# Kernel tuning notes

Hardware: AMD Instinct MI355X
Metric: run time of the kernel (lower is better)

Reference implementation:

```python
import jax, jax.numpy as jnp
import numpy as np

TEMPERATURE = 0.07


def setup_inputs() -> dict:
    key = jax.random.key(0)
    k1, k2, k3 = jax.random.split(key, 3)
    b, num_proposals, num_phrases, f = 128, 100, 16, 512
    img_features = jax.random.normal(k1, (b, num_proposals, f), dtype=jnp.float32)
    text_features = jax.random.normal(k2, (b, num_phrases, f), dtype=jnp.float32)
    labels = jax.random.randint(k3, (b, b), 0, 2, dtype=jnp.int64)
    return {"img_features": img_features, "text_features": text_features, "labels": labels}


def reference(img_features, text_features, labels):
    # att_matrix[b,d,t,i] = <text[b,t,:], img[d,i,:]>
    att_matrix = jnp.einsum('btf,dif->bdti', text_features, img_features)
    argmax_box = att_matrix.max(axis=3)        # [b, d, t]  max over proposals
    score_matrix = argmax_box.mean(axis=2)     # [b, d]     mean over phrases
    score_exp = jnp.exp(score_matrix / TEMPERATURE)
    return score_exp
```

## Files before the change

kernel.cpp:

```cpp
#include <hip/hip_runtime.h>
#include <hip/hip_bf16.h>
#include <stdint.h>


typedef __attribute__((ext_vector_type(8))) short bf16x8;
typedef __attribute__((ext_vector_type(4))) float f32x4;

constexpr int Bb = 128;
constexpr int P  = 100;
constexpr int T  = 16;
constexpr int F  = 512;
constexpr float TEMP = 0.07f;

constexpr int BM = 128;
constexpr int BN = 128;
constexpr int BK = 64;

__device__ __forceinline__ unsigned short f2bf(float x) {
  union { float f; uint32_t u; } c; c.f = x;
  uint32_t r = (c.u + 0x7FFFu + ((c.u >> 16) & 1u)) >> 16;
  return (unsigned short)r;
}

__global__ void cvt_kernel(const float4* __restrict__ img, const float4* __restrict__ txt,
                           ushort4* __restrict__ imgb, ushort4* __restrict__ txtb,
                           int nimg4, int ntxt4) {
  const int stride = gridDim.x * blockDim.x;
  for (int i = blockIdx.x * blockDim.x + threadIdx.x; i < nimg4; i += stride) {
    float4 v = img[i];
    ushort4 o = { f2bf(v.x), f2bf(v.y), f2bf(v.z), f2bf(v.w) };
    imgb[i] = o;
  }
  for (int i = blockIdx.x * blockDim.x + threadIdx.x; i < ntxt4; i += stride) {
    float4 v = txt[i];
    ushort4 o = { f2bf(v.x), f2bf(v.y), f2bf(v.z), f2bf(v.w) };
    txtb[i] = o;
  }
}

template<bool FUSED>
__global__ __launch_bounds__(256)
void score_kernel(const void* __restrict__ imgp, const void* __restrict__ txtp,
                  float* __restrict__ out) {
  __shared__ __align__(16) unsigned short As[BM * BK];
  __shared__ __align__(16) unsigned short Bs[BN * BK];
  __shared__ float red[BM][2];

  const int d    = blockIdx.x;
  const int b0   = blockIdx.y * (BM / T);
  const int tid  = threadIdx.x;
  const int lane = tid & 63;
  const int w    = tid >> 6;
  const int q    = lane >> 4;
  const int n    = lane & 15;
  const int mh   = w & 1;
  const int nh   = w >> 1;

  f32x4 acc[4][4] = {};

  for (int kk = 0; kk < F; kk += BK) {
    if constexpr (!FUSED) {
      const unsigned short* gi = (const unsigned short*)imgp;
      const unsigned short* gt = (const unsigned short*)txtp;
      const int sub = lane >> 3;
      const int col = (((lane & 7) ^ sub) & 7) * 8;
      #pragma unroll
      for (int rr = 0; rr < 4; rr++) {
        const int c   = rr * 4 + w;
        const int row = c * 8 + sub;
        const unsigned short* ga = gt + (size_t)(b0 * T + row) * F + kk + col;
        __builtin_amdgcn_global_load_lds(
            (const __attribute__((address_space(1))) void*)ga,
            (__attribute__((address_space(3))) void*)&As[c * 512], 16, 0, 0);
        const int prow = row < P ? row : 0;
        const unsigned short* gb = gi + ((size_t)d * P + prow) * F + kk + col;
        __builtin_amdgcn_global_load_lds(
            (const __attribute__((address_space(1))) void*)gb,
            (__attribute__((address_space(3))) void*)&Bs[c * 512], 16, 0, 0);
      }
    } else {
      const float* gi = (const float*)imgp;
      const float* gt = (const float*)txtp;
      #pragma unroll
      for (int s = 0; s < 8; s++) {
        const int slot = s * 256 + tid;
        const int row  = slot >> 4;
        const int half = slot & 15;
        const int colg = half * 4;
        const int kc   = half >> 1;
        const int cols = ((kc ^ (row & 7)) * 8) + (half & 1) * 4;
        float4 v = *(const float4*)(gt + (size_t)(b0 * T + row) * F + kk + colg);
        ushort4 o = { f2bf(v.x), f2bf(v.y), f2bf(v.z), f2bf(v.w) };
        *(ushort4*)&As[row * BK + cols] = o;
        const int prow = row < P ? row : 0;
        float4 u = *(const float4*)(gi + ((size_t)d * P + prow) * F + kk + colg);
        ushort4 p = { f2bf(u.x), f2bf(u.y), f2bf(u.z), f2bf(u.w) };
        *(ushort4*)&Bs[row * BK + cols] = p;
      }
    }
    __syncthreads();

    #pragma unroll
    for (int ks = 0; ks < 2; ks++) {
      const int kc = ks * 4 + q;
      const int sw = ((kc ^ (n & 7)) & 7) * 8;
      bf16x8 a[4], bb[4];
      #pragma unroll
      for (int rt = 0; rt < 4; rt++)
        a[rt] = *(const bf16x8*)&As[(mh * 64 + rt * 16 + n) * BK + sw];
      #pragma unroll
      for (int ct = 0; ct < 4; ct++)
        bb[ct] = *(const bf16x8*)&Bs[(nh * 64 + ct * 16 + n) * BK + sw];
      #pragma unroll
      for (int rt = 0; rt < 4; rt++)
        #pragma unroll
        for (int ct = 0; ct < 4; ct++)
          acc[rt][ct] = __builtin_amdgcn_mfma_f32_16x16x32_bf16(a[rt], bb[ct], acc[rt][ct], 0, 0, 0);
    }
    __syncthreads();
  }

  #pragma unroll
  for (int rt = 0; rt < 4; rt++) {
    float m[4];
    #pragma unroll
    for (int r = 0; r < 4; r++) {
      float v = -3.0e38f;
      #pragma unroll
      for (int ct = 0; ct < 4; ct++) {
        const bool valid = (nh * 64 + ct * 16 + n) < P;
        const float x = acc[rt][ct][r];
        v = valid ? fmaxf(v, x) : v;
      }
      #pragma unroll
      for (int off = 1; off < 16; off <<= 1)
        v = fmaxf(v, __shfl_xor(v, off));
      m[r] = v;
    }
    if (n == 0) {
      #pragma unroll
      for (int r = 0; r < 4; r++)
        red[mh * 64 + rt * 16 + q * 4 + r][nh] = m[r];
    }
  }
  __syncthreads();

  if (tid < BM / T) {
    float s = 0.f;
    #pragma unroll
    for (int t = 0; t < T; t++) {
      const int r = tid * T + t;
      s += fmaxf(red[r][0], red[r][1]);
    }
    const float arg = fminf(s * (1.0f / (T * TEMP)), 88.0f);
    out[(size_t)(b0 + tid) * Bb + d] = expf(arg);
  }
}

extern "C" void kernel_launch(void* const* d_in, const int* in_sizes, int n_in,
                              void* d_out, int out_size, void* d_ws, size_t ws_size,
                              hipStream_t stream) {
  const float* img = (const float*)d_in[0];
  const float* txt = (const float*)d_in[1];
  float* out = (float*)d_out;

  const size_t imgN = (size_t)Bb * P * F;
  const size_t txtN = (size_t)Bb * T * F;
  const size_t need = (imgN + txtN) * sizeof(unsigned short);

  dim3 grid(Bb, (Bb * T) / BM);
  if (ws_size >= need) {
    unsigned short* imgb = (unsigned short*)d_ws;
    unsigned short* txtb = imgb + imgN;
    cvt_kernel<<<2048, 256, 0, stream>>>((const float4*)img, (const float4*)txt,
                                         (ushort4*)imgb, (ushort4*)txtb,
                                         (int)(imgN / 4), (int)(txtN / 4));
    score_kernel<false><<<grid, 256, 0, stream>>>(imgb, txtb, out);
  } else {
    score_kernel<true><<<grid, 256, 0, stream>>>(img, txt, out);
  }
}
```

Before: 123.7 us.

## Switch GEMM operands from bf16 to fp8 with scaled 16x16x128 MFMA

Converts image and text features to FP8 (e4m3) instead of bf16 and uses the MI355X scaled f8f6f4 MFMA with K=128 per instruction. BK doubles to 128 bytes-equivalent layout, halving global/LDS traffic and MFMA count per K. This trades numerical accuracy: fp8 quantization of unit-normal data over a 512-length dot product may exceed the tolerance, especially after exp(score/0.07) amplifies errors.

```diff
diff --git a/kernel.cpp b/kernel.cpp
--- a/kernel.cpp
+++ b/kernel.cpp
@@ -3,7 +3,8 @@
 #include <stdint.h>
 
 
-typedef __attribute__((ext_vector_type(8))) short bf16x8;
+typedef __attribute__((ext_vector_type(4))) int   v4i;
+typedef __attribute__((ext_vector_type(8))) int   v8i;
 typedef __attribute__((ext_vector_type(4))) float f32x4;
 
 constexpr int Bb = 128;
@@ -13,28 +14,23 @@
 constexpr float TEMP = 0.07f;
 
 constexpr int BM = 128;
-constexpr int BN = 128;
-constexpr int BK = 64;
-
-__device__ __forceinline__ unsigned short f2bf(float x) {
-  union { float f; uint32_t u; } c; c.f = x;
-  uint32_t r = (c.u + 0x7FFFu + ((c.u >> 16) & 1u)) >> 16;
-  return (unsigned short)r;
-}
+constexpr int BK = 128;
 
 __global__ void cvt_kernel(const float4* __restrict__ img, const float4* __restrict__ txt,
-                           ushort4* __restrict__ imgb, ushort4* __restrict__ txtb,
+                           uint32_t* __restrict__ imgb, uint32_t* __restrict__ txtb,
                            int nimg4, int ntxt4) {
   const int stride = gridDim.x * blockDim.x;
   for (int i = blockIdx.x * blockDim.x + threadIdx.x; i < nimg4; i += stride) {
     float4 v = img[i];
-    ushort4 o = { f2bf(v.x), f2bf(v.y), f2bf(v.z), f2bf(v.w) };
-    imgb[i] = o;
+    int w = __builtin_amdgcn_cvt_pk_fp8_f32(v.x, v.y, 0, false);
+    w     = __builtin_amdgcn_cvt_pk_fp8_f32(v.z, v.w, w, true);
+    imgb[i] = (uint32_t)w;
   }
   for (int i = blockIdx.x * blockDim.x + threadIdx.x; i < ntxt4; i += stride) {
     float4 v = txt[i];
-    ushort4 o = { f2bf(v.x), f2bf(v.y), f2bf(v.z), f2bf(v.w) };
-    txtb[i] = o;
+    int w = __builtin_amdgcn_cvt_pk_fp8_f32(v.x, v.y, 0, false);
+    w     = __builtin_amdgcn_cvt_pk_fp8_f32(v.z, v.w, w, true);
+    txtb[i] = (uint32_t)w;
   }
 }
 
@@ -42,8 +38,8 @@
 __global__ __launch_bounds__(256)
 void score_kernel(const void* __restrict__ imgp, const void* __restrict__ txtp,
                   float* __restrict__ out) {
-  __shared__ __align__(16) unsigned short As[BM * BK];
-  __shared__ __align__(16) unsigned short Bs[BN * BK];
+  __shared__ __align__(16) unsigned char As[BM * BK];
+  __shared__ __align__(16) unsigned char Bs[BM * BK];
   __shared__ float red[BM][2];
 
   const int d    = blockIdx.x;
@@ -60,23 +56,23 @@
 
   for (int kk = 0; kk < F; kk += BK) {
     if constexpr (!FUSED) {
-      const unsigned short* gi = (const unsigned short*)imgp;
-      const unsigned short* gt = (const unsigned short*)txtp;
+      const uint8_t* gi = (const uint8_t*)imgp;
+      const uint8_t* gt = (const uint8_t*)txtp;
       const int sub = lane >> 3;
-      const int col = (((lane & 7) ^ sub) & 7) * 8;
+      const int col = (((lane & 7) ^ sub) & 7) * 16;
       #pragma unroll
       for (int rr = 0; rr < 4; rr++) {
         const int c   = rr * 4 + w;
         const int row = c * 8 + sub;
-        const unsigned short* ga = gt + (size_t)(b0 * T + row) * F + kk + col;
+        const uint8_t* ga = gt + (size_t)(b0 * T + row) * F + kk + col;
         __builtin_amdgcn_global_load_lds(
             (const __attribute__((address_space(1))) void*)ga,
-            (__attribute__((address_space(3))) void*)&As[c * 512], 16, 0, 0);
+            (__attribute__((address_space(3))) void*)&As[c * 1024], 16, 0, 0);
         const int prow = row < P ? row : 0;
-        const unsigned short* gb = gi + ((size_t)d * P + prow) * F + kk + col;
+        const uint8_t* gb = gi + ((size_t)d * P + prow) * F + kk + col;
         __builtin_amdgcn_global_load_lds(
             (const __attribute__((address_space(1))) void*)gb,
-            (__attribute__((address_space(3))) void*)&Bs[c * 512], 16, 0, 0);
+            (__attribute__((address_space(3))) void*)&Bs[c * 1024], 16, 0, 0);
       }
     } else {
       const float* gi = (const float*)imgp;
@@ -86,36 +82,52 @@
         const int slot = s * 256 + tid;
         const int row  = slot >> 4;
         const int half = slot & 15;
-        const int colg = half * 4;
-        const int kc   = half >> 1;
-        const int cols = ((kc ^ (row & 7)) * 8) + (half & 1) * 4;
-        float4 v = *(const float4*)(gt + (size_t)(b0 * T + row) * F + kk + colg);
-        ushort4 o = { f2bf(v.x), f2bf(v.y), f2bf(v.z), f2bf(v.w) };
-        *(ushort4*)&As[row * BK + cols] = o;
+        const int colf = half * 8;
+        const int swz  = ((half >> 1) ^ (row & 7));
+        const int offb = row * BK + swz * 16 + (half & 1) * 8;
+        float4 v0 = *(const float4*)(gt + (size_t)(b0 * T + row) * F + kk + colf);
+        float4 v1 = *(const float4*)(gt + (size_t)(b0 * T + row) * F + kk + colf + 4);
+        int w0 = __builtin_amdgcn_cvt_pk_fp8_f32(v0.x, v0.y, 0, false);
+        w0     = __builtin_amdgcn_cvt_pk_fp8_f32(v0.z, v0.w, w0, true);
+        int w1 = __builtin_amdgcn_cvt_pk_fp8_f32(v1.x, v1.y, 0, false);
+        w1     = __builtin_amdgcn_cvt_pk_fp8_f32(v1.z, v1.w, w1, true);
+        *(uint2*)&As[offb] = make_uint2((uint32_t)w0, (uint32_t)w1);
         const int prow = row < P ? row : 0;
-        float4 u = *(const float4*)(gi + ((size_t)d * P + prow) * F + kk + colg);
-        ushort4 p = { f2bf(u.x), f2bf(u.y), f2bf(u.z), f2bf(u.w) };
-        *(ushort4*)&Bs[row * BK + cols] = p;
+        float4 u0 = *(const float4*)(gi + ((size_t)d * P + prow) * F + kk + colf);
+        float4 u1 = *(const float4*)(gi + ((size_t)d * P + prow) * F + kk + colf + 4);
+        int x0 = __builtin_amdgcn_cvt_pk_fp8_f32(u0.x, u0.y, 0, false);
+        x0     = __builtin_amdgcn_cvt_pk_fp8_f32(u0.z, u0.w, x0, true);
+        int x1 = __builtin_amdgcn_cvt_pk_fp8_f32(u1.x, u1.y, 0, false);
+        x1     = __builtin_amdgcn_cvt_pk_fp8_f32(u1.z, u1.w, x1, true);
+        *(uint2*)&Bs[offb] = make_uint2((uint32_t)x0, (uint32_t)x1);
       }
     }
     __syncthreads();
 
-    #pragma unroll
-    for (int ks = 0; ks < 2; ks++) {
-      const int kc = ks * 4 + q;
-      const int sw = ((kc ^ (n & 7)) & 7) * 8;
-      bf16x8 a[4], bb[4];
+    {
+      const int k7 = n & 7;
+      const int s0 = (2 * q) ^ k7;
+      v8i a[4], bfr[4];
       #pragma unroll
-      for (int rt = 0; rt < 4; rt++)
-        a[rt] = *(const bf16x8*)&As[(mh * 64 + rt * 16 + n) * BK + sw];
+      for (int rt = 0; rt < 4; rt++) {
+        const int off = (mh * 64 + rt * 16 + n) * BK;
+        v4i lo = *(const v4i*)&As[off + s0 * 16];
+        v4i hi = *(const v4i*)&As[off + (s0 ^ 1) * 16];
+        a[rt] = __builtin_shufflevector(lo, hi, 0, 1, 2, 3, 4, 5, 6, 7);
+      }
       #pragma unroll
-      for (int ct = 0; ct < 4; ct++)
-        bb[ct] = *(const bf16x8*)&Bs[(nh * 64 + ct * 16 + n) * BK + sw];
+      for (int ct = 0; ct < 4; ct++) {
+        const int off = (nh * 64 + ct * 16 + n) * BK;
+        v4i lo = *(const v4i*)&Bs[off + s0 * 16];
+        v4i hi = *(const v4i*)&Bs[off + (s0 ^ 1) * 16];
+        bfr[ct] = __builtin_shufflevector(lo, hi, 0, 1, 2, 3, 4, 5, 6, 7);
+      }
       #pragma unroll
       for (int rt = 0; rt < 4; rt++)
         #pragma unroll
         for (int ct = 0; ct < 4; ct++)
-          acc[rt][ct] = __builtin_amdgcn_mfma_f32_16x16x32_bf16(a[rt], bb[ct], acc[rt][ct], 0, 0, 0);
+          acc[rt][ct] = __builtin_amdgcn_mfma_scale_f32_16x16x128_f8f6f4(
+              a[rt], bfr[ct], acc[rt][ct], 0, 0, 0, 127, 0, 127);
     }
     __syncthreads();
   }
@@ -166,14 +178,14 @@
 
   const size_t imgN = (size_t)Bb * P * F;
   const size_t txtN = (size_t)Bb * T * F;
-  const size_t need = (imgN + txtN) * sizeof(unsigned short);
+  const size_t need = imgN + txtN;
 
   dim3 grid(Bb, (Bb * T) / BM);
   if (ws_size >= need) {
-    unsigned short* imgb = (unsigned short*)d_ws;
-    unsigned short* txtb = imgb + imgN;
+    uint8_t* imgb = (uint8_t*)d_ws;
+    uint8_t* txtb = imgb + imgN;
     cvt_kernel<<<2048, 256, 0, stream>>>((const float4*)img, (const float4*)txt,
-                                         (ushort4*)imgb, (ushort4*)txtb,
+                                         (uint32_t*)imgb, (uint32_t*)txtb,
                                          (int)(imgN / 4), (int)(txtN / 4));
     score_kernel<false><<<grid, 256, 0, stream>>>(imgb, txtb, out);
   } else {
```

Result: faster. 103.7 us (-16.2%).
